# Optimization experiments

Hardware: AMD Instinct MI355X
Metric: run time of the kernel (lower is better)

## Reference

```python
import jax, jax.numpy as jnp
import numpy as np

N_ATOMS = 10000
N_PAIRS = 320000
C = 64        # channel width (pp_nodes[-1], ii_nodes[-1], pi_nodes[-1])
NB = 10       # n_basis
EPS = 1e-3    # torsion-boost epsilon


def setup_inputs() -> dict:
    key = jax.random.key(0)
    ks = jax.random.split(key, 24)
    f32 = jnp.float32

    def w(k, shp):
        return jax.random.normal(k, shp, f32) / np.float32(np.sqrt(shp[0]))

    ind_2 = jax.random.randint(ks[0], (N_PAIRS, 2), 0, N_ATOMS)
    p1 = jax.random.normal(ks[1], (N_ATOMS, C), f32)
    p3 = jax.random.normal(ks[2], (N_ATOMS, 3, C), f32)
    basis = jax.random.uniform(ks[3], (N_PAIRS, NB), dtype=f32)
    d3 = jax.random.normal(ks[4], (N_PAIRS, 3), f32)
    d3 = d3 / jnp.linalg.norm(d3, axis=-1, keepdims=True)  # unit bond directions
    fc_edge = jax.random.uniform(ks[5], (N_PAIRS, 1), dtype=f32)  # cutoff in [0,1]

    return {
        'ind_2': ind_2, 'p1': p1, 'p3': p3, 'basis': basis, 'd3': d3, 'fc_edge': fc_edge,
        'pp_pre_W1': w(ks[6], (C, C)), 'pp_pre_b1': jnp.zeros((C,), f32),
        'pp_pre_W2': w(ks[7], (C, C)), 'pp_pre_b2': jnp.zeros((C,), f32),
        'pi_W': w(ks[8], (2 * C, C * NB)), 'pi_b': jnp.zeros((C * NB,), f32),
        'ii_W': w(ks[9], (C, 2 * C)),
        'pp_post_W1': w(ks[10], (2 * C, C)), 'pp_post_W2': w(ks[11], (C, C)),
        'eq_pp_W': w(ks[12], (C, C)),
        'pp1_W1': w(ks[13], (2 * C, C)), 'pp1_b1': jnp.zeros((C,), f32),
        'pp1_W2': w(ks[14], (C, 2 * C)), 'pp1_b2': jnp.zeros((2 * C,), f32),
    }


def _gc_block(ind_2, p1, p3, basis, d3, fc_edge,
              pp_pre_W1, pp_pre_b1, pp_pre_W2, pp_pre_b2,
              pi_W, pi_b, ii_W, pp_post_W1, pp_post_W2,
              eq_pp_W, pp1_W1, pp1_b1, pp1_W2, pp1_b2):
    n_atoms = p1.shape[0]
    i = ind_2[:, 0]
    j = ind_2[:, 1]

    # ---- InvarLayer ----
    # pp_pre: FF [C,C], tanh, bias
    p1_in = jnp.tanh(jnp.tanh(p1 @ pp_pre_W1 + pp_pre_b1) @ pp_pre_W2 + pp_pre_b2)
    # PILayer: concat(p1[i], p1[j]) -> Dense(C*NB) -> contract with radial basis
    pair = jnp.concatenate([p1_in[i], p1_in[j]], axis=-1)            # (P, 2C)
    h = jnp.tanh(pair @ pi_W + pi_b).reshape(-1, C, NB)              # (P, C, NB)
    i_pair = jnp.einsum('pcb,pb->pc', h, basis)                      # (P, C)
    # ii: FF [2C] (doubled for n_props=2), tanh, no bias
    i_pair = jnp.tanh(i_pair @ ii_W)                                 # (P, 2C)
    # IP: scatter-add onto receiver atom i
    p1_scat = jax.ops.segment_sum(i_pair, i, num_segments=n_atoms)   # (N, 2C)
    # pp_post: FF [C,C], tanh, no bias
    p1_new = jnp.tanh(jnp.tanh(p1_scat @ pp_post_W1) @ pp_post_W2)   # (N, C)

    i1a, i1b = jnp.split(i_pair, 2, axis=-1)  # chunks; rank-3 branch uses i1s[1]

    # ---- torsion boost (compute_torsion_boost_t3) ----
    v = jax.ops.segment_sum(d3 * fc_edge, i, num_segments=n_atoms)   # (N, 3)
    v_i = v[i]
    proj = jnp.sum(v_i * d3, axis=-1, keepdims=True)
    w = v_i - proj * d3                                              # perpendicular part
    w2 = jnp.sum(w * w, axis=-1, keepdims=True)
    g_deg = w2 / (w2 + (10.0 * EPS) ** 2)
    t3 = w * jax.lax.rsqrt(w2 + EPS * EPS) * g_deg                   # (P, 3)
    tb_gate = g_deg * (fc_edge * fc_edge)                            # (P, 1)

    # ---- EquivarLayer ----
    gate = i1b[:, None, :]                                           # (P, 1, C)
    ix = p3[j] * gate + d3[:, :, None] * gate \
         + t3[:, :, None] * (i1b * tb_gate)[:, None, :]              # (P, 3, C)
    p3_new = jax.ops.segment_sum(ix, i, num_segments=n_atoms)        # (N, 3, C)
    p3_new = p3_new @ eq_pp_W                                        # PP: no bias, no act
    dotted = jnp.einsum('ixr,ixr->ir', p3_new, p3_new)               # (N, C)

    # ---- output PP + gating ----
    h2 = jnp.tanh(jnp.concatenate([p1_new, dotted], axis=-1) @ pp1_W1 + pp1_b1)
    h2 = jnp.tanh(h2 @ pp1_W2 + pp1_b2)                              # (N, 2C)
    g1, g3 = jnp.split(h2, 2, axis=-1)
    p1_out = g1                                                      # (N, C)
    p3_out = p3_new * g3[:, None, :]                                 # ScaleLayer
    return p1_out, p3_out


def reference(ind_2, p1, p3, basis, d3, fc_edge,
              pp_pre_W1, pp_pre_b1, pp_pre_W2, pp_pre_b2,
              pi_W, pi_b, ii_W, pp_post_W1, pp_post_W2,
              eq_pp_W, pp1_W1, pp1_b1, pp1_W2, pp1_b2):
    return _gc_block(ind_2, p1, p3, basis, d3, fc_edge,
                     pp_pre_W1, pp_pre_b1, pp_pre_W2, pp_pre_b2,
                     pi_W, pi_b, ii_W, pp_post_W1, pp_post_W2,
                     eq_pp_W, pp1_W1, pp1_b1, pp1_W2, pp1_b2)
```

## Files before the change

### kernel.cpp

```cpp
#include <hip/hip_runtime.h>
#include <hip/hip_bf16.h>

#define N_ATOMS 10000
#define N_PAIRS 320000
#define C_ 64
#define NB_ 10

typedef short bf16x8 __attribute__((ext_vector_type(8)));
typedef float f32x4 __attribute__((ext_vector_type(4)));

__device__ __forceinline__ float bf2f(__hip_bfloat16 x) { return __bfloat162float(x); }
__device__ __forceinline__ float ldf(const void* p, int i, int isf32) {
    return isf32 ? ((const float*)p)[i] : bf2f(((const __hip_bfloat16*)p)[i]);
}
__device__ __forceinline__ short f2bs(float x) {
    __hip_bfloat16 h = __float2bfloat16(x);
    return *reinterpret_cast<short*>(&h);
}
__device__ __forceinline__ float bs2f(unsigned short s) {
    return __uint_as_float(((unsigned)s) << 16);
}
__device__ __forceinline__ float tanh_fast(float x) {
    const float e = __expf(2.0f * x);
    return 1.0f - 2.0f * __builtin_amdgcn_rcpf(e + 1.0f);
}

#define W_PPREW1 0
#define W_PPREB1 4096
#define W_PPREW2 4160
#define W_PPREB2 8256
#define W_PIW    8320
#define W_PIB    90240
#define W_IIW    90880
#define W_PPOSTW1 99072
#define W_PPOSTW2 107264
#define W_EQW    111360
#define W_Q1W    115456
#define W_Q1B    123648
#define W_Q2W    123712
#define W_Q2B    131904
#define W_TOTAL  132032

__global__ void k_probe(const void* __restrict__ d3, int* __restrict__ flag)
{
    if (threadIdx.x == 0 && blockIdx.x == 0) {
        float sf = 0.f, sb = 0.f;
        const float* f = (const float*)d3;
        const __hip_bfloat16* b = (const __hip_bfloat16*)d3;
        for (int r = 0; r < 4; r++) {
            float x = f[r*3], y = f[r*3+1], z = f[r*3+2];
            float n = x*x + y*y + z*z;
            sf += isfinite(n) ? fabsf(n - 1.f) : 1e30f;
            float xb = bf2f(b[r*3]), yb = bf2f(b[r*3+1]), zb = bf2f(b[r*3+2]);
            float nb = xb*xb + yb*yb + zb*zb;
            sb += isfinite(nb) ? fabsf(nb - 1.f) : 1e30f;
        }
        *flag = (sf < sb) ? 1 : 0;
    }
}

__global__ __launch_bounds__(256) void k_convert(
    const void* s0, const void* s1, const void* s2, const void* s3,
    const void* s4, const void* s5, const void* s6, const void* s7,
    const void* s8, const void* s9, const void* s10, const void* s11,
    const void* s12, const void* s13,
    float* __restrict__ wbuf, const int* __restrict__ flagp)
{
    const int idx = blockIdx.x * 256 + threadIdx.x;
    if (idx >= W_TOTAL) return;
    const int isf32 = *flagp;
    const int offs[15] = {W_PPREW1, W_PPREB1, W_PPREW2, W_PPREB2, W_PIW, W_PIB,
                          W_IIW, W_PPOSTW1, W_PPOSTW2, W_EQW, W_Q1W, W_Q1B,
                          W_Q2W, W_Q2B, W_TOTAL};
    const void* srcs[14] = {s0,s1,s2,s3,s4,s5,s6,s7,s8,s9,s10,s11,s12,s13};
    int t = 0;
    while (idx >= offs[t + 1]) t++;
    wbuf[idx] = ldf(srcs[t], idx - offs[t], isf32);
}

__global__ __launch_bounds__(256) void k_prep(
    const float* __restrict__ wbuf,
    short* __restrict__ piWB2,
    short* __restrict__ iiWh, short* __restrict__ iiWl,
    const void* __restrict__ p1, const int* __restrict__ flagp,
    unsigned short* __restrict__ p1h, unsigned short* __restrict__ p1l)
{
    __shared__ float x[4][C_];
    __shared__ float h[4][C_];
    if (blockIdx.x < 352) {
        int idx = blockIdx.x * 256 + threadIdx.x;
        if (idx < 81920) {
            const int j = idx & 7, lane = (idx >> 3) & 63, s = (idx >> 9) & 3, T = idx >> 11;
            const int k = s * 32 + (lane >> 4) * 8 + j;
            const int colp = T * 16 + (lane & 15);
            const int b = colp >> 6, c = colp & 63;
            const float v = wbuf[W_PIW + k * 640 + c * 10 + b];
            const short hs = f2bs(v);
            const int cc = idx >> 13, e = idx & 8191;
            piWB2[cc * 16384 + e] = hs;
            piWB2[cc * 16384 + 8192 + e] = f2bs(v - bs2f((unsigned short)hs));
            return;
        }
        idx -= 81920;
        if (idx < 8192) {
            const int j = idx & 7, lane = (idx >> 3) & 63, s2 = (idx >> 9) & 1, ct = idx >> 10;
            const int k = s2 * 32 + (lane >> 4) * 8 + j;
            const int col = ct * 16 + (lane & 15);
            const float wv = wbuf[W_IIW + k * 128 + col];
            const short hs = f2bs(wv);
            iiWh[idx] = hs;
            iiWl[idx] = f2bs(wv - bs2f((unsigned short)hs));
        }
        return;
    }
    const float* W1 = wbuf + W_PPREW1;
    const float* b1 = wbuf + W_PPREB1;
    const float* W2 = wbuf + W_PPREW2;
    const float* b2 = wbuf + W_PPREB2;
    const int isf32 = *flagp;
    const int t = threadIdx.x;
    const int slot = t >> 6, c = t & 63;
    const int atom = (blockIdx.x - 352) * 4 + slot;
    x[slot][c] = ldf(p1, atom * C_ + c, isf32);
    __syncthreads();
    float acc = b1[c];
    for (int k = 0; k < C_; k++) acc += x[slot][k] * W1[k * C_ + c];
    h[slot][c] = tanh_fast(acc);
    __syncthreads();
    acc = b2[c];
    for (int k = 0; k < C_; k++) acc += h[slot][k] * W2[k * C_ + c];
    const float f = tanh_fast(acc);
    const short hs = f2bs(f);
    p1h[atom * C_ + c] = (unsigned short)hs;
    p1l[atom * C_ + c] = (unsigned short)f2bs(f - bs2f((unsigned short)hs));
}

__global__ __launch_bounds__(256) void k_hist(const int* __restrict__ ind2, int* __restrict__ cnt)
{
    const int p = blockIdx.x * 256 + threadIdx.x;
    if (p < N_PAIRS) atomicAdd(&cnt[ind2[2 * p]], 1);
}
__global__ __launch_bounds__(256) void k_scan(const int* __restrict__ cnt,
                                              int* __restrict__ offs, int* __restrict__ cur)
{
    __shared__ int part[256];
    __shared__ int base[257];
    const int t = threadIdx.x;
    const int lo = t * 40, hi = (lo + 40 < N_ATOMS) ? lo + 40 : N_ATOMS;
    int s = 0;
    for (int b = lo; b < hi; b++) s += cnt[b];
    part[t] = s;
    __syncthreads();
    if (t == 0) {
        int run = 0;
        for (int i = 0; i < 256; i++) { base[i] = run; run += part[i]; }
        base[256] = run;
    }
    __syncthreads();
    int run = base[t];
    for (int b = lo; b < hi; b++) { offs[b] = run; cur[b] = run; run += cnt[b]; }
    if (t == 0) offs[N_ATOMS] = base[256];
}
__global__ __launch_bounds__(256) void k_scatter(const int* __restrict__ ind2,
                                                 int* __restrict__ cur, int* __restrict__ perm)
{
    const int p = blockIdx.x * 256 + threadIdx.x;
    if (p >= N_PAIRS) return;
    const int pos = atomicAdd(&cur[ind2[2 * p]], 1);
    perm[pos] = p;
}

__global__ __launch_bounds__(256) void k_gatherperm(
    const int* __restrict__ ind2, const void* __restrict__ basis,
    const void* __restrict__ d3, const void* __restrict__ fc,
    const int* __restrict__ perm, const int* __restrict__ flagp,
    int* __restrict__ ind2P, float* __restrict__ basisP,
    float* __restrict__ d3P, float* __restrict__ fcP, float* __restrict__ v)
{
    const int q = blockIdx.x * 256 + threadIdx.x;
    if (q >= N_PAIRS) return;
    const int isf32 = *flagp;
    const int p = perm[q];
    const int2 ij = ((const int2*)ind2)[p];
    ((int2*)ind2P)[q] = ij;
    const float f = ldf(fc, p, isf32);
    fcP[q] = f;
    float dd[3];
    #pragma unroll
    for (int x = 0; x < 3; x++) {
        dd[x] = ldf(d3, 3 * p + x, isf32);
        d3P[3 * q + x] = dd[x];
    }
    #pragma unroll
    for (int x = 0; x < 3; x++) atomicAdd(&v[ij.x * 3 + x], dd[x] * f);
    #pragma unroll
    for (int b = 0; b < 10; b++) basisP[10 * q + b] = ldf(basis, 10 * p + b, isf32);
}

__global__ __launch_bounds__(256) void k_pairs_fused(
    const int* __restrict__ ind2P, const float* __restrict__ basisP,
    const float* __restrict__ d3P, const float* __restrict__ fcP,
    const void* __restrict__ p3,
    const float* __restrict__ wbuf,
    const short* __restrict__ piWB2,
    const short* __restrict__ iiWh, const short* __restrict__ iiWl,
    const unsigned short* __restrict__ p1h, const unsigned short* __restrict__ p1l,
    const int* __restrict__ flagp, const float* __restrict__ vglob,
    float* __restrict__ p1scat, float* __restrict__ p3acc)
{
    __shared__ __align__(16) char SH[33280];
    __shared__ float basisL[640];
    __shared__ float biasT[640];
    __shared__ int sIL[65], sJL[64];
    __shared__ float d3L[64][3], t3L[64][3], tbL[64];

    unsigned short* Bbuf = (unsigned short*)SH;
    float* preL = (float*)SH;
    float* ipL  = (float*)SH;

    const int t = threadIdx.x;
    const int P0 = blockIdx.x * 64;
    const int isf32 = *flagp;
    const int lane = t & 63;
    const int w = t >> 6;
    const int lc = lane & 15;
    const int quad = lane >> 4;

    if (t < 64) {
        int2 ij = ((const int2*)ind2P)[P0 + t];
        sIL[t] = ij.x; sJL[t] = ij.y;
        const float vi0 = vglob[ij.x * 3 + 0], vi1 = vglob[ij.x * 3 + 1], vi2 = vglob[ij.x * 3 + 2];
        const float d0 = d3P[(P0 + t) * 3 + 0];
        const float d1 = d3P[(P0 + t) * 3 + 1];
        const float d2 = d3P[(P0 + t) * 3 + 2];
        d3L[t][0] = d0; d3L[t][1] = d1; d3L[t][2] = d2;
        const float proj = vi0 * d0 + vi1 * d1 + vi2 * d2;
        const float w0 = vi0 - proj * d0, w1 = vi1 - proj * d1, w2v = vi2 - proj * d2;
        const float w2 = w0 * w0 + w1 * w1 + w2v * w2v;
        const float g = w2 / (w2 + 1e-4f);
        const float rs = rsqrtf(w2 + 1e-6f);
        t3L[t][0] = w0 * rs * g; t3L[t][1] = w1 * rs * g; t3L[t][2] = w2v * rs * g;
        const float f = fcP[P0 + t];
        tbL[t] = g * f * f;
    }
    if (t == 64) sIL[64] = -1;
    for (int e = t; e < 640; e += 256) basisL[e] = basisP[P0 * 10 + e];
    for (int e = t; e < 640; e += 256) biasT[e] = wbuf[W_PIB + (e & 63) * 10 + (e >> 6)];
    __syncthreads();

    bf16x8 ah[4], al[4];
    {
        const int ia = sIL[w * 16 + lc];
        const int ja = sJL[w * 16 + lc];
        #pragma unroll
        for (int s = 0; s < 4; s++) {
            const int atom = (s < 2) ? ia : ja;
            const int off = atom * 64 + (s & 1) * 32 + quad * 8;
            ah[s] = *(const bf16x8*)(p1h + off);
            al[s] = *(const bf16x8*)(p1l + off);
        }
    }

    float sr[4][4];
    #pragma unroll
    for (int r = 0; r < 4; r++)
        #pragma unroll
        for (int ph = 0; ph < 4; ph++) sr[r][ph] = 0.f;

    for (int cc = 0; cc < 10; cc++) {
        if (cc) __syncthreads();
        {
            const uint4* gsrc = (const uint4*)(piWB2 + cc * 16384);
            uint4* ldst = (uint4*)Bbuf;
            #pragma unroll
            for (int r = 0; r < 8; r++) ldst[r * 256 + t] = gsrc[r * 256 + t];
        }
        __syncthreads();
        #pragma unroll
        for (int tt = 0; tt < 4; tt++) {
            f32x4 acc = {0.f, 0.f, 0.f, 0.f};
            #pragma unroll
            for (int s = 0; s < 4; s++) {
                const int e = ((tt * 4 + s) * 64 + lane) * 8;
                bf16x8 bh = *(const bf16x8*)&Bbuf[e];
                bf16x8 bl = *(const bf16x8*)&Bbuf[8192 + e];
                acc = __builtin_amdgcn_mfma_f32_16x16x32_bf16(ah[s], bh, acc, 0, 0, 0);
                acc = __builtin_amdgcn_mfma_f32_16x16x32_bf16(al[s], bh, acc, 0, 0, 0);
                acc = __builtin_amdgcn_mfma_f32_16x16x32_bf16(ah[s], bl, acc, 0, 0, 0);
            }
            const float bias = biasT[cc * 64 + tt * 16 + lc];
            #pragma unroll
            for (int r = 0; r < 4; r++) {
                const int m = w * 16 + quad * 4 + r;
                const float h = tanh_fast(acc[r] + bias);
                sr[r][tt] += h * basisL[m * 10 + cc];
            }
        }
    }
    __syncthreads();

    #pragma unroll
    for (int r = 0; r < 4; r++)
        #pragma unroll
        for (int ph = 0; ph < 4; ph++)
            preL[(w * 16 + quad * 4 + r) * 68 + ph * 16 + lc] = sr[r][ph];
    __syncthreads();

    bf16x8 ah2[2], al2[2];
    {
        const int row = w * 16 + lc;
        #pragma unroll
        for (int s2 = 0; s2 < 2; s2++) {
            const float* pr2 = &preL[row * 68 + s2 * 32 + quad * 8];
            #pragma unroll
            for (int j = 0; j < 8; j++) {
                const float x = pr2[j];
                const short hs = f2bs(x);
                ah2[s2][j] = hs;
                al2[s2][j] = f2bs(x - bs2f((unsigned short)hs));
            }
        }
    }
    __syncthreads();

    float pv0[16];
    if (t < 192) {
        #pragma unroll
        for (int u = 0; u < 16; u++) pv0[u] = ldf(p3, sJL[u] * 192 + t, isf32);
    }

    #pragma unroll
    for (int ct = 0; ct < 8; ct++) {
        f32x4 acc = {0.f, 0.f, 0.f, 0.f};
        #pragma unroll
        for (int s2 = 0; s2 < 2; s2++) {
            bf16x8 bh = *(const bf16x8*)&iiWh[((ct * 2 + s2) * 64 + lane) * 8];
            bf16x8 bl = *(const bf16x8*)&iiWl[((ct * 2 + s2) * 64 + lane) * 8];
            acc = __builtin_amdgcn_mfma_f32_16x16x32_bf16(ah2[s2], bh, acc, 0, 0, 0);
            acc = __builtin_amdgcn_mfma_f32_16x16x32_bf16(al2[s2], bh, acc, 0, 0, 0);
            acc = __builtin_amdgcn_mfma_f32_16x16x32_bf16(ah2[s2], bl, acc, 0, 0, 0);
        }
        const int ch = ct * 16 + lc;
        #pragma unroll
        for (int r = 0; r < 4; r++) {
            const int m = w * 16 + quad * 4 + r;
            ipL[m * 130 + ch] = tanh_fast(acc[r]);
        }
    }
    __syncthreads();

    if (t < 192) {
        const int x = t >> 6, cc2 = t & 63;
        float acc = 0.f;
        #pragma unroll
        for (int blk = 0; blk < 4; blk++) {
            float pv[16];
            if (blk == 0) {
                #pragma unroll
                for (int u = 0; u < 16; u++) pv[u] = pv0[u];
            } else {
                #pragma unroll
                for (int u = 0; u < 16; u++)
                    pv[u] = ldf(p3, sJL[blk * 16 + u] * 192 + t, isf32);
            }
            #pragma unroll
            for (int u = 0; u < 16; u++) {
                const int m = blk * 16 + u;
                const float ipb = ipL[m * 130 + 64 + cc2];
                acc += (pv[u] + d3L[m][x]) * ipb + t3L[m][x] * (ipb * tbL[m]);
                if (sIL[m + 1] != sIL[m]) {
                    atomicAdd(&p3acc[(size_t)sIL[m] * 192 + t], acc);
                    acc = 0.f;
                }
            }
        }
    } else {
        const int ch0 = t - 192;
        float a0 = 0.f, a1 = 0.f;
        #pragma unroll 8
        for (int m = 0; m < 64; m++) {
            a0 += ipL[m * 130 + ch0];
            a1 += ipL[m * 130 + 64 + ch0];
            if (sIL[m + 1] != sIL[m]) {
                const size_t base = (size_t)sIL[m] * 128;
                atomicAdd(&p1scat[base + ch0], a0);
                atomicAdd(&p1scat[base + 64 + ch0], a1);
                a0 = 0.f; a1 = 0.f;
            }
        }
    }
}

__global__ __launch_bounds__(256) void k_pairs_atomic(
    const int* __restrict__ ind2, const void* __restrict__ basis,
    const void* __restrict__ d3, const void* __restrict__ fc,
    const void* __restrict__ p3,
    const float* __restrict__ wbuf,
    const short* __restrict__ piWB2,
    const short* __restrict__ iiWh, const short* __restrict__ iiWl,
    const unsigned short* __restrict__ p1h, const unsigned short* __restrict__ p1l,
    const int* __restrict__ flagp, const float* __restrict__ vglob,
    float* __restrict__ outA, float* __restrict__ outB)
{
    __shared__ __align__(16) unsigned short Bbuf[8192];
    __shared__ __align__(16) char SH[17408];
    __shared__ float basisL[640];
    __shared__ int sIL[64], sJL[64];
    __shared__ float d3L[64][3], t3L[64][3], tbL[64];

    float* preL = (float*)SH;
    float* i1bL = (float*)SH;

    const int t = threadIdx.x;
    const int P0 = blockIdx.x * 64;
    const int isf32 = *flagp;
    const int lane = t & 63;
    const int w = t >> 6;
    const int lc = lane & 15;
    const int quad = lane >> 4;

    if (t < 64) {
        int2 ij = ((const int2*)ind2)[P0 + t];
        sIL[t] = ij.x; sJL[t] = ij.y;
    }
    for (int e = t; e < 640; e += 256) basisL[e] = ldf(basis, P0 * 10 + e, isf32);
    __syncthreads();

    bf16x8 ah[4], al[4];
    {
        const int ia = sIL[w * 16 + lc];
        const int ja = sJL[w * 16 + lc];
        #pragma unroll
        for (int s = 0; s < 4; s++) {
            const int atom = (s < 2) ? ia : ja;
            const int off = atom * 64 + (s & 1) * 32 + quad * 8;
            ah[s] = *(const bf16x8*)(p1h + off);
            al[s] = *(const bf16x8*)(p1l + off);
        }
    }

    float sr[4][4];
    #pragma unroll
    for (int r = 0; r < 4; r++)
        #pragma unroll
        for (int ph = 0; ph < 4; ph++) sr[r][ph] = 0.f;

    for (int cc = 0; cc < 10; cc++) {
        f32x4 acc[4];
        #pragma unroll
        for (int tt = 0; tt < 4; tt++) acc[tt] = (f32x4){0.f, 0.f, 0.f, 0.f};

        __syncthreads();
        {
            const uint4* gsrc = (const uint4*)(piWB2 + cc * 16384);
            uint4* ldst = (uint4*)Bbuf;
            #pragma unroll
            for (int r = 0; r < 4; r++) ldst[r * 256 + t] = gsrc[r * 256 + t];
        }
        __syncthreads();
        #pragma unroll
        for (int tt = 0; tt < 4; tt++) {
            #pragma unroll
            for (int s = 0; s < 4; s++) {
                bf16x8 bfr = *(const bf16x8*)&Bbuf[((tt * 4 + s) * 64 + lane) * 8];
                acc[tt] = __builtin_amdgcn_mfma_f32_16x16x32_bf16(ah[s], bfr, acc[tt], 0, 0, 0);
                acc[tt] = __builtin_amdgcn_mfma_f32_16x16x32_bf16(al[s], bfr, acc[tt], 0, 0, 0);
            }
        }
        __syncthreads();
        {
            const uint4* gsrc = (const uint4*)(piWB2 + cc * 16384 + 8192);
            uint4* ldst = (uint4*)Bbuf;
            #pragma unroll
            for (int r = 0; r < 4; r++) ldst[r * 256 + t] = gsrc[r * 256 + t];
        }
        __syncthreads();
        #pragma unroll
        for (int tt = 0; tt < 4; tt++) {
            #pragma unroll
            for (int s = 0; s < 4; s++) {
                bf16x8 bfr = *(const bf16x8*)&Bbuf[((tt * 4 + s) * 64 + lane) * 8];
                acc[tt] = __builtin_amdgcn_mfma_f32_16x16x32_bf16(ah[s], bfr, acc[tt], 0, 0, 0);
            }
            const int c = tt * 16 + lc;
            const float bias = wbuf[W_PIB + c * 10 + cc];
            #pragma unroll
            for (int r = 0; r < 4; r++) {
                const int m = w * 16 + quad * 4 + r;
                const float h = tanh_fast(acc[tt][r] + bias);
                sr[r][tt] += h * basisL[m * 10 + cc];
            }
        }
    }

    #pragma unroll
    for (int r = 0; r < 4; r++)
        #pragma unroll
        for (int ph = 0; ph < 4; ph++)
            preL[(w * 16 + quad * 4 + r) * 68 + ph * 16 + lc] = sr[r][ph];
    __syncthreads();

    bf16x8 ah2[2], al2[2];
    {
        const int row = w * 16 + lc;
        #pragma unroll
        for (int s2 = 0; s2 < 2; s2++) {
            const float* pr2 = &preL[row * 68 + s2 * 32 + quad * 8];
            #pragma unroll
            for (int j = 0; j < 8; j++) {
                const float x = pr2[j];
                const short hs = f2bs(x);
                ah2[s2][j] = hs;
                al2[s2][j] = f2bs(x - bs2f((unsigned short)hs));
            }
        }
    }
    __syncthreads();

    #pragma unroll
    for (int ct = 0; ct < 8; ct++) {
        f32x4 acc = {0.f, 0.f, 0.f, 0.f};
        #pragma unroll
        for (int s2 = 0; s2 < 2; s2++) {
            bf16x8 bh = *(const bf16x8*)&iiWh[((ct * 2 + s2) * 64 + lane) * 8];
            bf16x8 bl = *(const bf16x8*)&iiWl[((ct * 2 + s2) * 64 + lane) * 8];
            acc = __builtin_amdgcn_mfma_f32_16x16x32_bf16(ah2[s2], bh, acc, 0, 0, 0);
            acc = __builtin_amdgcn_mfma_f32_16x16x32_bf16(al2[s2], bh, acc, 0, 0, 0);
            acc = __builtin_amdgcn_mfma_f32_16x16x32_bf16(ah2[s2], bl, acc, 0, 0, 0);
        }
        const int ch = ct * 16 + lc;
        #pragma unroll
        for (int r = 0; r < 4; r++) {
            const int m = w * 16 + quad * 4 + r;
            const float val = tanh_fast(acc[r]);
            atomicAdd(&outA[(size_t)sIL[m] * 128 + ch], val);
            if (ch >= 64) i1bL[m * 64 + (ch - 64)] = val;
        }
    }

    __syncthreads();
    if (t < 64) {
        const int m = t;
        const int ia = sIL[m];
        const float vi0 = vglob[ia * 3 + 0], vi1 = vglob[ia * 3 + 1], vi2 = vglob[ia * 3 + 2];
        const float d0 = ldf(d3, (P0 + m) * 3 + 0, isf32);
        const float d1 = ldf(d3, (P0 + m) * 3 + 1, isf32);
        const float d2 = ldf(d3, (P0 + m) * 3 + 2, isf32);
        d3L[m][0] = d0; d3L[m][1] = d1; d3L[m][2] = d2;
        const float proj = vi0 * d0 + vi1 * d1 + vi2 * d2;
        const float w0 = vi0 - proj * d0, w1 = vi1 - proj * d1, w2v = vi2 - proj * d2;
        const float w2 = w0 * w0 + w1 * w1 + w2v * w2v;
        const float g = w2 / (w2 + 1e-4f);
        const float rs = rsqrtf(w2 + 1e-6f);
        t3L[m][0] = w0 * rs * g; t3L[m][1] = w1 * rs * g; t3L[m][2] = w2v * rs * g;
        const float f = ldf(fc, P0 + m, isf32);
        tbL[m] = g * f * f;
    }
    __syncthreads();
    const int c = lane;
    #pragma unroll 4
    for (int mm = 0; mm < 16; mm++) {
        const int m = w * 16 + mm;
        const float bv = i1bL[m * 64 + c];
        const float coef = bv * tbL[m];
        #pragma unroll
        for (int x = 0; x < 3; x++) {
            const float p3v = ldf(p3, sJL[m] * 192 + x * 64 + c, isf32);
            atomicAdd(&outB[(size_t)sIL[m] * 192 + x * 64 + c],
                      p3v * bv + d3L[m][x] * bv + t3L[m][x] * coef);
        }
    }
}

__global__ __launch_bounds__(256) void k_final(
    const float* __restrict__ p1scat, const float* __restrict__ p3acc,
    const float* __restrict__ wbuf, const int* __restrict__ flagp,
    void* __restrict__ out)
{
    const float* ppW1 = wbuf + W_PPOSTW1;
    const float* ppW2 = wbuf + W_PPOSTW2;
    const float* eqW  = wbuf + W_EQW;
    const float* q1W  = wbuf + W_Q1W;
    const float* q1b  = wbuf + W_Q1B;
    const float* q2W  = wbuf + W_Q2W;
    const float* q2b  = wbuf + W_Q2B;
    const int isf32 = *flagp;

    __shared__ float s1[4][128];
    __shared__ float hA[4][64];
    __shared__ float cat[4][128];
    __shared__ float p3a[4][192];
    const int t = threadIdx.x;
    const int slot = t >> 6, c = t & 63;
    const int atom = blockIdx.x * 4 + slot;

    s1[slot][c]        = p1scat[atom * 128 + c];
    s1[slot][64 + c]   = p1scat[atom * 128 + 64 + c];
    p3a[slot][c]       = p3acc[atom * 192 + c];
    p3a[slot][64 + c]  = p3acc[atom * 192 + 64 + c];
    p3a[slot][128 + c] = p3acc[atom * 192 + 128 + c];
    __syncthreads();

    float acc = 0.f;
    for (int k = 0; k < 128; k++) acc += s1[slot][k] * ppW1[k * 64 + c];
    hA[slot][c] = tanh_fast(acc);
    __syncthreads();
    acc = 0.f;
    for (int k = 0; k < 64; k++) acc += hA[slot][k] * ppW2[k * 64 + c];
    cat[slot][c] = tanh_fast(acc);

    float pn[3];
    float dot = 0.f;
    #pragma unroll
    for (int x = 0; x < 3; x++) {
        float a = 0.f;
        for (int k = 0; k < 64; k++) a += p3a[slot][x * 64 + k] * eqW[k * 64 + c];
        pn[x] = a;
        dot += a * a;
    }
    cat[slot][64 + c] = dot;
    __syncthreads();

    acc = q1b[c];
    for (int k = 0; k < 128; k++) acc += cat[slot][k] * q1W[k * 64 + c];
    __syncthreads();
    hA[slot][c] = tanh_fast(acc);
    __syncthreads();

    float g1acc = q2b[c], g3acc = q2b[c + 64];
    for (int k = 0; k < 64; k++) {
        const float hv = hA[slot][k];
        g1acc += hv * q2W[k * 128 + c];
        g3acc += hv * q2W[k * 128 + c + 64];
    }
    const float g1 = tanh_fast(g1acc);
    const float g3 = tanh_fast(g3acc);
    if (isf32) {
        float* p1o = (float*)out;
        float* p3o = p1o + 640000;
        p1o[atom * 64 + c] = g1;
        #pragma unroll
        for (int x = 0; x < 3; x++) p3o[atom * 192 + x * 64 + c] = pn[x] * g3;
    } else {
        __hip_bfloat16* p1o = (__hip_bfloat16*)out;
        __hip_bfloat16* p3o = p1o + 640000;
        p1o[atom * 64 + c] = __float2bfloat16(g1);
        #pragma unroll
        for (int x = 0; x < 3; x++) p3o[atom * 192 + x * 64 + c] = __float2bfloat16(pn[x] * g3);
    }
}

__global__ __launch_bounds__(256) void k_vscat(
    const int* __restrict__ ind2, const void* __restrict__ d3,
    const void* __restrict__ fc, const int* __restrict__ flagp, float* __restrict__ v)
{
    const int p = blockIdx.x * 256 + threadIdx.x;
    if (p >= N_PAIRS) return;
    const int isf32 = *flagp;
    const int ia = ind2[2 * p];
    const float f = ldf(fc, p, isf32);
    atomicAdd(&v[ia * 3 + 0], ldf(d3, p * 3 + 0, isf32) * f);
    atomicAdd(&v[ia * 3 + 1], ldf(d3, p * 3 + 1, isf32) * f);
    atomicAdd(&v[ia * 3 + 2], ldf(d3, p * 3 + 2, isf32) * f);
}

extern "C" void kernel_launch(void* const* d_in, const int* in_sizes, int n_in,
                              void* d_out, int out_size, void* d_ws, size_t ws_size,
                              hipStream_t stream)
{
    const int* ind2 = (const int*)d_in[0];
    const void* p1    = d_in[1];
    const void* p3    = d_in[2];
    const void* basis = d_in[3];
    const void* d3    = d_in[4];
    const void* fc    = d_in[5];

    char* W = (char*)d_ws;
    float* wbuf  = (float*)(W + 0);
    short* piWB2 = (short*)(W + 528128);
    short* iiWh  = (short*)(W + 1183488);
    short* iiWl  = (short*)(W + 1199872);
    unsigned short* p1h = (unsigned short*)(W + 1216256);
    unsigned short* p1l = (unsigned short*)(W + 2496256);
    int* flag = (int*)(W + 3776256);

    const int fused = (ws_size >= 38576384ULL) ? 1 : 0;

    k_probe<<<1, 64, 0, stream>>>(d3, flag);

    if (fused) {
        int* offs     = (int*)(W + 3776320);
        int* cur      = (int*)(W + 3816384);
        int* perm     = (int*)(W + 3856384);
        int* ind2P    = (int*)(W + 5136384);
        float* basisP = (float*)(W + 7696384);
        float* d3P    = (float*)(W + 20496384);
        float* fcP    = (float*)(W + 24336384);
        int* cnt      = (int*)(W + 25616384);
        float* v      = (float*)(W + 25656384);
        float* p1scat = (float*)(W + 25776384);
        float* p3acc  = (float*)(W + 30896384);

        hipMemsetAsync(cnt, 0, 40000 + 120000 + 5120000 + 7680000, stream);
        k_convert<<<516, 256, 0, stream>>>(
            d_in[6], d_in[7], d_in[8], d_in[9], d_in[10], d_in[11], d_in[12],
            d_in[13], d_in[14], d_in[15], d_in[16], d_in[17], d_in[18], d_in[19],
            wbuf, flag);
        k_prep<<<2852, 256, 0, stream>>>(wbuf, piWB2, iiWh, iiWl, p1, flag, p1h, p1l);
        k_hist<<<1250, 256, 0, stream>>>(ind2, cnt);
        k_scan<<<1, 256, 0, stream>>>(cnt, offs, cur);
        k_scatter<<<1250, 256, 0, stream>>>(ind2, cur, perm);
        k_gatherperm<<<1250, 256, 0, stream>>>(ind2, basis, d3, fc, perm, flag,
                                               ind2P, basisP, d3P, fcP, v);
        k_pairs_fused<<<5000, 256, 0, stream>>>(ind2P, basisP, d3P, fcP, p3,
                                                wbuf, piWB2, iiWh, iiWl,
                                                p1h, p1l, flag, v, p1scat, p3acc);
        k_final<<<2500, 256, 0, stream>>>(p1scat, p3acc, wbuf, flag, d_out);
    } else {
        float* v      = (float*)(W + 3776320);
        float* p1scat = (float*)(W + 3896320);
        float* p3acc  = (float*)(W + 9016320);

        hipMemsetAsync(v, 0, 120000 + 5120000 + 7680000, stream);
        k_convert<<<516, 256, 0, stream>>>(
            d_in[6], d_in[7], d_in[8], d_in[9], d_in[10], d_in[11], d_in[12],
            d_in[13], d_in[14], d_in[15], d_in[16], d_in[17], d_in[18], d_in[19],
            wbuf, flag);
        k_prep<<<2852, 256, 0, stream>>>(wbuf, piWB2, iiWh, iiWl, p1, flag, p1h, p1l);
        k_vscat<<<1250, 256, 0, stream>>>(ind2, d3, fc, flag, v);
        k_pairs_atomic<<<5000, 256, 0, stream>>>(ind2, basis, d3, fc, p3,
                                                 wbuf, piWB2, iiWh, iiWl,
                                                 p1h, p1l, flag, v,
                                                 p1scat, p3acc);
        k_final<<<2500, 256, 0, stream>>>(p1scat, p3acc, wbuf, flag, d_out);
    }
}
```

Before: 565.0 us.

## Merge setup kernels, prefetch PI weights into registers, remap block order

Folds the probe into the histogram kernel, the scan into the weight-convert kernel, and the scatter into the prep kernel, removing several small launches. In the fused pair kernel, the next PI-weight chunk is prefetched into registers while the current chunk is used, so global loads overlap with MFMA work. Blocks are also remapped across 8 strided groups. The prefetch costs extra VGPRs (8 uint4 per thread), which may lower occupancy. The mixed kernels still rely on stream order between dependent stages, and the combined scan block does its serial work alongside the convert blocks.

```diff
diff --git a/kernel.cpp b/kernel.cpp
--- a/kernel.cpp
+++ b/kernel.cpp
@@ -41,52 +41,94 @@
 #define W_Q2B    131904
 #define W_TOTAL  132032
 
+__device__ __forceinline__ void probe_body(const void* d3, int* flag)
+{
+    float sf = 0.f, sb = 0.f;
+    const float* f = (const float*)d3;
+    const __hip_bfloat16* b = (const __hip_bfloat16*)d3;
+    for (int r = 0; r < 4; r++) {
+        float x = f[r*3], y = f[r*3+1], z = f[r*3+2];
+        float n = x*x + y*y + z*z;
+        sf += isfinite(n) ? fabsf(n - 1.f) : 1e30f;
+        float xb = bf2f(b[r*3]), yb = bf2f(b[r*3+1]), zb = bf2f(b[r*3+2]);
+        float nb = xb*xb + yb*yb + zb*zb;
+        sb += isfinite(nb) ? fabsf(nb - 1.f) : 1e30f;
+    }
+    *flag = (sf < sb) ? 1 : 0;
+}
+
 __global__ void k_probe(const void* __restrict__ d3, int* __restrict__ flag)
 {
-    if (threadIdx.x == 0 && blockIdx.x == 0) {
-        float sf = 0.f, sb = 0.f;
-        const float* f = (const float*)d3;
-        const __hip_bfloat16* b = (const __hip_bfloat16*)d3;
-        for (int r = 0; r < 4; r++) {
-            float x = f[r*3], y = f[r*3+1], z = f[r*3+2];
-            float n = x*x + y*y + z*z;
-            sf += isfinite(n) ? fabsf(n - 1.f) : 1e30f;
-            float xb = bf2f(b[r*3]), yb = bf2f(b[r*3+1]), zb = bf2f(b[r*3+2]);
-            float nb = xb*xb + yb*yb + zb*zb;
-            sb += isfinite(nb) ? fabsf(nb - 1.f) : 1e30f;
-        }
-        *flag = (sf < sb) ? 1 : 0;
-    }
-}
-
-__global__ __launch_bounds__(256) void k_convert(
+    if (threadIdx.x == 0 && blockIdx.x == 0) probe_body(d3, flag);
+}
+
+__global__ __launch_bounds__(256) void k_probe_hist(
+    const void* __restrict__ d3, int* __restrict__ flag,
+    const int* __restrict__ ind2, int* __restrict__ cnt)
+{
+    if (blockIdx.x == 0 && threadIdx.x == 0) probe_body(d3, flag);
+    const int p = blockIdx.x * 256 + threadIdx.x;
+    if (p < N_PAIRS) atomicAdd(&cnt[ind2[2 * p]], 1);
+}
+
+__global__ __launch_bounds__(256) void k_convert_scan(
     const void* s0, const void* s1, const void* s2, const void* s3,
     const void* s4, const void* s5, const void* s6, const void* s7,
     const void* s8, const void* s9, const void* s10, const void* s11,
     const void* s12, const void* s13,
-    float* __restrict__ wbuf, const int* __restrict__ flagp)
-{
-    const int idx = blockIdx.x * 256 + threadIdx.x;
-    if (idx >= W_TOTAL) return;
-    const int isf32 = *flagp;
-    const int offs[15] = {W_PPREW1, W_PPREB1, W_PPREW2, W_PPREB2, W_PIW, W_PIB,
-                          W_IIW, W_PPOSTW1, W_PPOSTW2, W_EQW, W_Q1W, W_Q1B,
-                          W_Q2W, W_Q2B, W_TOTAL};
-    const void* srcs[14] = {s0,s1,s2,s3,s4,s5,s6,s7,s8,s9,s10,s11,s12,s13};
-    int t = 0;
-    while (idx >= offs[t + 1]) t++;
-    wbuf[idx] = ldf(srcs[t], idx - offs[t], isf32);
-}
-
-__global__ __launch_bounds__(256) void k_prep(
+    float* __restrict__ wbuf, const int* __restrict__ flagp,
+    const int* __restrict__ cnt, int* __restrict__ offs, int* __restrict__ cur)
+{
+    __shared__ int part[256];
+    __shared__ int base[257];
+    if (blockIdx.x < 516) {
+        const int idx = blockIdx.x * 256 + threadIdx.x;
+        if (idx >= W_TOTAL) return;
+        const int isf32 = *flagp;
+        const int offw[15] = {W_PPREW1, W_PPREB1, W_PPREW2, W_PPREB2, W_PIW, W_PIB,
+                              W_IIW, W_PPOSTW1, W_PPOSTW2, W_EQW, W_Q1W, W_Q1B,
+                              W_Q2W, W_Q2B, W_TOTAL};
+        const void* srcs[14] = {s0,s1,s2,s3,s4,s5,s6,s7,s8,s9,s10,s11,s12,s13};
+        int t = 0;
+        while (idx >= offw[t + 1]) t++;
+        wbuf[idx] = ldf(srcs[t], idx - offw[t], isf32);
+        return;
+    }
+    const int t = threadIdx.x;
+    const int lo = t * 40, hi = (lo + 40 < N_ATOMS) ? lo + 40 : N_ATOMS;
+    int s = 0;
+    for (int b = lo; b < hi; b++) s += cnt[b];
+    part[t] = s;
+    __syncthreads();
+    if (t == 0) {
+        int run = 0;
+        for (int i = 0; i < 256; i++) { base[i] = run; run += part[i]; }
+        base[256] = run;
+    }
+    __syncthreads();
+    int run = base[t];
+    for (int b = lo; b < hi; b++) { offs[b] = run; cur[b] = run; run += cnt[b]; }
+    if (t == 0) offs[N_ATOMS] = base[256];
+}
+
+__global__ __launch_bounds__(256) void k_prep_scatter(
     const float* __restrict__ wbuf,
     short* __restrict__ piWB2,
     short* __restrict__ iiWh, short* __restrict__ iiWl,
     const void* __restrict__ p1, const int* __restrict__ flagp,
-    unsigned short* __restrict__ p1h, unsigned short* __restrict__ p1l)
+    unsigned short* __restrict__ p1h, unsigned short* __restrict__ p1l,
+    const int* __restrict__ ind2, int* __restrict__ cur, int* __restrict__ perm)
 {
     __shared__ float x[4][C_];
     __shared__ float h[4][C_];
+    if (blockIdx.x >= 2852) {
+        const int p = (blockIdx.x - 2852) * 256 + threadIdx.x;
+        if (p < N_PAIRS) {
+            const int pos = atomicAdd(&cur[ind2[2 * p]], 1);
+            perm[pos] = p;
+        }
+        return;
+    }
     if (blockIdx.x < 352) {
         int idx = blockIdx.x * 256 + threadIdx.x;
         if (idx < 81920) {
@@ -135,41 +177,6 @@
     p1l[atom * C_ + c] = (unsigned short)f2bs(f - bs2f((unsigned short)hs));
 }
 
-__global__ __launch_bounds__(256) void k_hist(const int* __restrict__ ind2, int* __restrict__ cnt)
-{
-    const int p = blockIdx.x * 256 + threadIdx.x;
-    if (p < N_PAIRS) atomicAdd(&cnt[ind2[2 * p]], 1);
-}
-__global__ __launch_bounds__(256) void k_scan(const int* __restrict__ cnt,
-                                              int* __restrict__ offs, int* __restrict__ cur)
-{
-    __shared__ int part[256];
-    __shared__ int base[257];
-    const int t = threadIdx.x;
-    const int lo = t * 40, hi = (lo + 40 < N_ATOMS) ? lo + 40 : N_ATOMS;
-    int s = 0;
-    for (int b = lo; b < hi; b++) s += cnt[b];
-    part[t] = s;
-    __syncthreads();
-    if (t == 0) {
-        int run = 0;
-        for (int i = 0; i < 256; i++) { base[i] = run; run += part[i]; }
-        base[256] = run;
-    }
-    __syncthreads();
-    int run = base[t];
-    for (int b = lo; b < hi; b++) { offs[b] = run; cur[b] = run; run += cnt[b]; }
-    if (t == 0) offs[N_ATOMS] = base[256];
-}
-__global__ __launch_bounds__(256) void k_scatter(const int* __restrict__ ind2,
-                                                 int* __restrict__ cur, int* __restrict__ perm)
-{
-    const int p = blockIdx.x * 256 + threadIdx.x;
-    if (p >= N_PAIRS) return;
-    const int pos = atomicAdd(&cur[ind2[2 * p]], 1);
-    perm[pos] = p;
-}
-
 __global__ __launch_bounds__(256) void k_gatherperm(
     const int* __restrict__ ind2, const void* __restrict__ basis,
     const void* __restrict__ d3, const void* __restrict__ fc,
@@ -219,12 +226,20 @@
     float* ipL  = (float*)SH;
 
     const int t = threadIdx.x;
-    const int P0 = blockIdx.x * 64;
+    const int bid = blockIdx.x;
+    const int P0 = ((bid & 7) * 625 + (bid >> 3)) * 64;
     const int isf32 = *flagp;
     const int lane = t & 63;
     const int w = t >> 6;
     const int lc = lane & 15;
     const int quad = lane >> 4;
+
+    uint4 stg[8];
+    {
+        const uint4* g = (const uint4*)piWB2;
+        #pragma unroll
+        for (int r = 0; r < 8; r++) stg[r] = g[r * 256 + t];
+    }
 
     if (t < 64) {
         int2 ij = ((const int2*)ind2P)[P0 + t];
@@ -268,14 +283,17 @@
         for (int ph = 0; ph < 4; ph++) sr[r][ph] = 0.f;
 
     for (int cc = 0; cc < 10; cc++) {
-        if (cc) __syncthreads();
         {
-            const uint4* gsrc = (const uint4*)(piWB2 + cc * 16384);
             uint4* ldst = (uint4*)Bbuf;
             #pragma unroll
-            for (int r = 0; r < 8; r++) ldst[r * 256 + t] = gsrc[r * 256 + t];
+            for (int r = 0; r < 8; r++) ldst[r * 256 + t] = stg[r];
         }
         __syncthreads();
+        if (cc < 9) {
+            const uint4* g = (const uint4*)(piWB2 + (cc + 1) * 16384);
+            #pragma unroll
+            for (int r = 0; r < 8; r++) stg[r] = g[r * 256 + t];
+        }
         #pragma unroll
         for (int tt = 0; tt < 4; tt++) {
             f32x4 acc = {0.f, 0.f, 0.f, 0.f};
@@ -296,8 +314,8 @@
                 sr[r][tt] += h * basisL[m * 10 + cc];
             }
         }
-    }
-    __syncthreads();
+        __syncthreads();
+    }
 
     #pragma unroll
     for (int r = 0; r < 4; r++)
@@ -686,8 +704,6 @@
 
     const int fused = (ws_size >= 38576384ULL) ? 1 : 0;
 
-    k_probe<<<1, 64, 0, stream>>>(d3, flag);
-
     if (fused) {
         int* offs     = (int*)(W + 3776320);
         int* cur      = (int*)(W + 3816384);
@@ -702,14 +718,13 @@
         float* p3acc  = (float*)(W + 30896384);
 
         hipMemsetAsync(cnt, 0, 40000 + 120000 + 5120000 + 7680000, stream);
-        k_convert<<<516, 256, 0, stream>>>(
+        k_probe_hist<<<1250, 256, 0, stream>>>(d3, flag, ind2, cnt);
+        k_convert_scan<<<517, 256, 0, stream>>>(
             d_in[6], d_in[7], d_in[8], d_in[9], d_in[10], d_in[11], d_in[12],
             d_in[13], d_in[14], d_in[15], d_in[16], d_in[17], d_in[18], d_in[19],
-            wbuf, flag);
-        k_prep<<<2852, 256, 0, stream>>>(wbuf, piWB2, iiWh, iiWl, p1, flag, p1h, p1l);
-        k_hist<<<1250, 256, 0, stream>>>(ind2, cnt);
-        k_scan<<<1, 256, 0, stream>>>(cnt, offs, cur);
-        k_scatter<<<1250, 256, 0, stream>>>(ind2, cur, perm);
+            wbuf, flag, cnt, offs, cur);
+        k_prep_scatter<<<4102, 256, 0, stream>>>(wbuf, piWB2, iiWh, iiWl, p1, flag,
+                                                 p1h, p1l, ind2, cur, perm);
         k_gatherperm<<<1250, 256, 0, stream>>>(ind2, basis, d3, fc, perm, flag,
                                                ind2P, basisP, d3P, fcP, v);
         k_pairs_fused<<<5000, 256, 0, stream>>>(ind2P, basisP, d3P, fcP, p3,
@@ -722,11 +737,13 @@
         float* p3acc  = (float*)(W + 9016320);
 
         hipMemsetAsync(v, 0, 120000 + 5120000 + 7680000, stream);
-        k_convert<<<516, 256, 0, stream>>>(
+        k_probe<<<1, 64, 0, stream>>>(d3, flag);
+        k_convert_scan<<<516, 256, 0, stream>>>(
             d_in[6], d_in[7], d_in[8], d_in[9], d_in[10], d_in[11], d_in[12],
             d_in[13], d_in[14], d_in[15], d_in[16], d_in[17], d_in[18], d_in[19],
-            wbuf, flag);
-        k_prep<<<2852, 256, 0, stream>>>(wbuf, piWB2, iiWh, iiWl, p1, flag, p1h, p1l);
+            wbuf, flag, nullptr, nullptr, nullptr);
+        k_prep_scatter<<<2852, 256, 0, stream>>>(wbuf, piWB2, iiWh, iiWl, p1, flag,
+                                                 p1h, p1l, nullptr, nullptr, nullptr);
         k_vscat<<<1250, 256, 0, stream>>>(ind2, d3, fc, flag, v);
         k_pairs_atomic<<<5000, 256, 0, stream>>>(ind2, basis, d3, fc, p3,
                                                  wbuf, piWB2, iiWh, iiWl,
```

Result: slower. 851.1 us (+50.6%).
